# Kernel tuning notes

Hardware: AMD Instinct MI355X
Metric: run time of the kernel (lower is better)

Reference implementation:

```python
import jax, jax.numpy as jnp
import numpy as np
import math

T, P, ITERS, H = 6, 8, 2, 8          # nr_types, num_proto, iters, n_head
D, F = 512, 1024                      # dim_proto, feature_dim (hidden_dim==D)
L = T * ITERS                         # 12 cross-attention layers


def _ln(x, g=None, b=None, eps=1e-5):
    m = x.mean(-1, keepdims=True)
    v = x.var(-1, keepdims=True)
    y = (x - m) * jax.lax.rsqrt(v + eps)
    if g is not None:
        y = y * g + b
    return y


def _forward(x_batch, batch_mask, node_type, pm_W, pm_b, pm_g, pm_bn,
             proto_logsigma, rand_mul, Wq, bq, Wk, bk, Wv, bv, Wo, bo,
             ag, ab, Wm1, bm1, lg, lb, Wm2, bm2, pg, pb):
    B, N, _ = x_batch.shape
    dt = x_batch.dtype
    bm = batch_mask.astype(dt)                                   # [B,N]
    onehot = jax.nn.one_hot(node_type, T, dtype=dt)              # [B,N,T]
    valid = bm * jnp.any(x_batch != 0, axis=-1).astype(dt)       # [B,N]
    mbt = onehot * valid[:, :, None]                             # [B,N,T]
    sums = jnp.einsum('bnt,bnf->btf', mbt, x_batch)              # per-(batch,type) sum
    cnt = mbt.sum(1)                                             # [B,T]
    fallback = x_batch.sum(1) / bm.sum(1, keepdims=True)         # [B,F]
    proto_mu = jnp.where(cnt[..., None] > 0,
                         sums / jnp.maximum(cnt, 1.0)[..., None],
                         fallback[:, None, :])                   # [B,T,F]

    # proto_mlp: Linear + LayerNorm + GELU (dropout = eval/identity)
    mu = jax.nn.gelu(_ln(proto_mu @ pm_W + pm_b, pm_g, pm_bn), approximate=False)  # [B,T,D]
    all_proto = mu[:, :, None, :] + jnp.exp(proto_logsigma)[None] * rand_mul[None]  # [B,T,P,D]

    dh = D // H
    scale = 1.0 / math.sqrt(dh)
    keymask = bm[:, None, None, :] == 0                          # [B,1,1,N]

    def layer(q, i):
        resid = q                                                 # [B,P,D]
        k = _ln((x_batch @ Wk[i] + bk[i]).reshape(B, N, H, dh))   # QK-LayerNorm (no affine)
        v = (x_batch @ Wv[i] + bv[i]).reshape(B, N, H, dh)
        qh = _ln((q @ Wq[i] + bq[i]).reshape(B, P, H, dh))
        dots = jnp.einsum('bkhd,bnhd->bkhn', qh, k) * scale       # [B,P,H,N]
        dots = jnp.where(keymask, -jnp.inf, dots)
        attn = jax.nn.softmax(dots, axis=-1)
        upd = jnp.einsum('bnhd,bkhn->bkhd', v, attn).reshape(B, P, D)
        upd = upd @ Wo[i] + bo[i]
        q = resid + _ln(upd, ag[i], ab[i])
        h = jax.nn.gelu(_ln(q @ Wm1[i] + bm1[i], lg[i], lb[i]), approximate=False)
        h = h @ Wm2[i] + bm2[i]
        return q + _ln(h, pg[i], pb[i])

    outs = []
    c = 0
    for i in range(T):
        p = all_proto[:, i]
        for _ in range(ITERS):
            p = layer(p, c)
            c += 1
        outs.append(p)
    prototypes = jnp.stack(outs, axis=1)                          # [B,T,P,D]
    return prototypes, proto_mu


def setup_inputs() -> dict:
    key = jax.random.key(0)
    ks = jax.random.split(key, 40)
    B, N = 4, 4096
    sc = 0.02

    def rn(i, shape, s=sc):
        return jax.random.normal(ks[i], shape, jnp.float32) * s

    inp = {
        'x_batch': jax.random.normal(ks[0], (B, N, F), jnp.float32),
        'batch_mask': jax.random.randint(ks[1], (B, N), 0, 2, jnp.int32),
        'node_type': jax.random.randint(ks[2], (B, N), 0, T, jnp.int32),
        'pm_W': rn(3, (F, D)), 'pm_b': jnp.zeros((D,)),
        'pm_g': jnp.ones((D,)), 'pm_bn': jnp.zeros((D,)),
        'proto_logsigma': rn(4, (T, 1, D), 0.05),
        'rand_mul': jax.random.normal(ks[5], (T, P, D), jnp.float32),
        'Wq': rn(6, (L, D, D)), 'bq': jnp.zeros((L, D)),
        'Wk': rn(7, (L, F, D)), 'bk': jnp.zeros((L, D)),
        'Wv': rn(8, (L, F, D)), 'bv': jnp.zeros((L, D)),
        'Wo': rn(9, (L, D, D)), 'bo': jnp.zeros((L, D)),
        'ag': jnp.ones((L, D)), 'ab': jnp.zeros((L, D)),
        'Wm1': rn(10, (L, D, D)), 'bm1': jnp.zeros((L, D)),
        'lg': jnp.ones((L, D)), 'lb': jnp.zeros((L, D)),
        'Wm2': rn(11, (L, D, D)), 'bm2': jnp.zeros((L, D)),
        'pg': jnp.ones((L, D)), 'pb': jnp.zeros((L, D)),
    }
    return inp


def reference(x_batch, batch_mask, node_type, pm_W, pm_b, pm_g, pm_bn,
              proto_logsigma, rand_mul, Wq, bq, Wk, bk, Wv, bv, Wo, bo,
              ag, ab, Wm1, bm1, lg, lb, Wm2, bm2, pg, pb):
    return _forward(x_batch, batch_mask, node_type, pm_W, pm_b, pm_g, pm_bn,
                    proto_logsigma, rand_mul, Wq, bq, Wk, bk, Wv, bv, Wo, bo,
                    ag, ab, Wm1, bm1, lg, lb, Wm2, bm2, pg, pb)
```

## Files before the change

### kernel.cpp

```cpp
#include <hip/hip_runtime.h>
#include <hip/hip_bf16.h>
#include <stdint.h>

#define TT 6
#define PP 8
#define HH 8
#define DD 512
#define FF 1024
#define DH 64
#define NB 4
#define NN 4096
#define LL 12
#define NCH 16
#define CHK 256

typedef __attribute__((ext_vector_type(8))) short short8v;
typedef __attribute__((ext_vector_type(4))) float f32x4;
typedef __attribute__((ext_vector_type(4))) unsigned short u16x4;
typedef __attribute__((ext_vector_type(8))) unsigned short u16x8;
typedef unsigned short u16;

__device__ __forceinline__ float bf2f(u16 u){
  union { unsigned int i; float f; } x; x.i = ((unsigned int)u) << 16; return x.f;
}
// ... 224 lines not shown
    pref[0] = 0;
    for (int j = 0; j < 256; ++j) pref[j+1] = pref[j] + csum[j];
  }
  __syncthreads();
  int off = b*NN + pref[tid];
  #pragma unroll
  for (int i = 0; i < 16; ++i){ if (f[i]) nidx[off++] = tid*16 + i; }
  if (tid == 0) cntc[b] = pref[256];
}

__global__ void k_wbfT(const void* __restrict__ Wq, const void* __restrict__ Wo,
                       const void* __restrict__ Wm1, const void* __restrict__ Wm2,
                       u16* __restrict__ Wt, const int* __restrict__ flagp){
  int f32 = *flagp;
  int z = blockIdx.z;
  int fam = z / LL;
  const void* src = (fam==0) ? Wq : (fam==1) ? Wo : (fam==2) ? Wm1 : Wm2;
  size_t sbase = (size_t)(z % LL) * DD * DD;
  __shared__ u16 tile[32][33];
  int d0 = blockIdx.x*32, k0 = blockIdx.y*32;
  int tx = threadIdx.x, ty = threadIdx.y;
  #pragma unroll
  for (int i = 0; i < 4; ++i){
    size_t idx = sbase + (size_t)(k0 + ty + i*8)*DD + d0 + tx;
    u16 v;
    if (f32) v = f2bf(((const float*)src)[idx]);
    else     v = ((const u16*)src)[idx];
    tile[ty + i*8][tx] = v;
  }
  __syncthreads();
  #pragma unroll
  for (int i = 0; i < 4; ++i)
    Wt[((size_t)z*DD + d0 + ty + i*8)*DD + k0 + tx] = tile[tx][ty + i*8];
}

__global__ void __launch_bounds__(512) k_mu(const float* __restrict__ colsums,
   const float* __restrict__ coltotal, const float* __restrict__ cnt,
   const float* __restrict__ bmsum,
   const void* __restrict__ pmWx, const void* __restrict__ pmb,
   const void* __restrict__ pmg, const void* __restrict__ pmbn,
   const void* __restrict__ lsig, const void* __restrict__ rmul,
   float* __restrict__ qstate, void* __restrict__ dout, int wmode,
   const int* __restrict__ flagp){
  int f32 = *flagp;
  int wf32 = wmode ? f32 : 0;
  const size_t OFFP = (size_t)NB*TT*PP*DD;
  int bt = blockIdx.x; int b = bt/TT, t = bt%TT;
  int d = threadIdx.x;
  __shared__ float xs[FF];
  __shared__ float red[4096];
  __shared__ float r1[8], r2[8];
  float cv = cnt[bt];
  float inv = 1.f / fmaxf(cv, 1.f);
  float fbinv = 1.f / bmsum[b];
  #pragma unroll
  for (int h = 0; h < 2; ++h){
    int f = d + h*512;
    float pm = (cv > 0.f) ? colsums[(size_t)bt*FF + f] * inv
                          : coltotal[b*FF + f] * fbinv;
    xs[f] = pm;
    if (f32) ((float*)dout)[OFFP + (size_t)bt*FF + f] = pm;
    else     ((u16*)dout)[OFFP + (size_t)bt*FF + f] = f2bf(pm);
  }
  __syncthreads();
  float acc = ldf(pmb, d, f32) + gemv_vec(xs, pmWx, 0, FF, wf32, red, d);
  int lane = d & 63, wid = d >> 6;
  float s1 = wave_sum(acc), s2 = wave_sum(acc*acc);
  if (lane==0){ r1[wid]=s1; r2[wid]=s2; }
  __syncthreads();
  float m=0, qq=0;
  #pragma unroll
  for (int i=0;i<8;++i){ m+=r1[i]; qq+=r2[i]; }
  m *= (1.f/DD); float var = qq*(1.f/DD) - m*m;
  float y = (acc - m) * rsqrtf(var + 1e-5f) * ldf(pmg, d, f32) + ldf(pmbn, d, f32);
  float mu = 0.5f * y * (1.f + erff(y * 0.70710678118654752f));
  #pragma unroll
  for (int p = 0; p < PP; ++p){
    float rv = ldf(rmul, (size_t)(t*PP+p)*DD + d, f32);
    float ls = ldf(lsig, (size_t)t*DD + d, f32);
    qstate[(((size_t)(b*TT+t))*PP + p)*DD + d] = mu + expf(ls) * rv;
  }
}

__global__ void k_transpose(const void* __restrict__ Wk, const void* __restrict__ Wv,
                            u16* __restrict__ TK, u16* __restrict__ TV,
                            int tlo, int s, const int* __restrict__ flagp){
  int f32 = *flagp;
  int ti = blockIdx.z >> 1, kv = blockIdx.z & 1;
  int c = 2*(tlo+ti)+s;
  size_t eoff = (size_t)c*FF*DD;
  const void* W = kv ? Wv : Wk;
  u16* T = (kv ? TV : TK) + (size_t)ti*FF*DD;
  __shared__ u16 tile[32][33];
  int n0 = blockIdx.x * 32, k0 = blockIdx.y * 32;
  int tx = threadIdx.x, ty = threadIdx.y;
  #pragma unroll
  for (int i = 0; i < 4; ++i){
    size_t idx = eoff + (size_t)(k0 + ty + i*8)*DD + n0 + tx;
    u16 v;
    if (f32) v = f2bf(((const float*)W)[idx]);
    else     v = ((const u16*)W)[idx];
    tile[ty + i*8][tx] = v;
  }
  __syncthreads();
  #pragma unroll
  for (int i = 0; i < 4; ++i)
    T[(size_t)(n0 + ty + i*8)*FF + k0 + tx] = tile[tx][ty + i*8];
}

__global__ void __launch_bounds__(512) k_kvgemm(const u16* __restrict__ Xb,
    const u16* __restrict__ TK, const u16* __restrict__ TV,
    const void* __restrict__ bk, const void* __restrict__ bv,
    u16* __restrict__ Kb, u16* __restrict__ Vb,
    const int* __restrict__ nidx, const int* __restrict__ cntc,
    int tlo, int s, int nt, const int* __restrict__ flagp){
  int f32 = *flagp;
  int orig = blockIdx.x;
  int x = orig & 7, r = orig >> 3;
  int bx = r / nt, pr = r - bx*nt;
  int pairg = x*nt + pr;
  int by = pairg & 3; int kvti = pairg >> 2; int kv = kvti & 1; int ti = kvti >> 1;
  int b = bx >> 4, jt = bx & 15;
  int cnt = cntc[b];
  if (jt*256 >= cnt) return;
  int c = 2*(tlo+ti)+s;
  size_t boff = (size_t)c*DD;
  const u16* WT = (kv ? TV : TK) + (size_t)ti*FF*DD;
  const void* bias = kv ? bv : bk;
  u16* out = (kv ? Vb : Kb) + (size_t)ti*((size_t)NB*NN*DD);
  int n0 = by*128;
  __shared__ __align__(16) char LDS[3*24576];
  int tid = threadIdx.x, wid = tid >> 6, lane = tid & 63;
  int wr = wid >> 1, wcn = wid & 1;
  const u16* gp0; const u16* gp1; const u16* gp2;
  int lo0, lo1, lo2;
  {
    const u16* gps[3]; int los[3];
    #pragma unroll
    for (int i = 0; i < 3; ++i){
      int e = tid + i*512;
      if (e < 1024){
        int row = e>>2, sp = e&3;
        int ssrc = sp ^ (((row>>3)&1)<<1);
        int cl = jt*256 + row; if (cl >= cnt) cl = cnt-1;
        int grow = nidx[b*NN + cl];
        gps[i] = Xb + ((size_t)b*NN + grow)*FF + ssrc*8;
        los[i] = e*16;
      } else {
        int e2 = e - 1024;
        int row = e2>>2, sp = e2&3;
        int ssrc = sp ^ (((row>>3)&1)<<1);
        gps[i] = WT + (size_t)(n0 + row)*FF + ssrc*8;
        los[i] = 16384 + e2*16;
      }
    }
    gp0=gps[0]; gp1=gps[1]; gp2=gps[2];
    lo0=los[0]; lo1=los[1]; lo2=los[2];
  }
#define STAGE(T) { char* bb_ = LDS + ((T)%3)*24576; \
  glds16(gp0 + (T)*32, bb_ + lo0); glds16(gp1 + (T)*32, bb_ + lo1); \
  glds16(gp2 + (T)*32, bb_ + lo2); }
  int ke = (lane>>4) ^ (((lane>>3)&1)<<1);
  int arow[4], brow[4];
  #pragma unroll
  for (int mi = 0; mi < 4; ++mi)
    arow[mi] = (wr*64 + mi*16 + (lane&15))*64 + ke*16;
  #pragma unroll
  for (int ni = 0; ni < 4; ++ni)
    brow[ni] = 16384 + (wcn*64 + ni*16 + (lane&15))*64 + ke*16;
  f32x4 acc[4][4] = {};
  STAGE(0);
  STAGE(1);
  asm volatile("s_waitcnt vmcnt(3)" ::: "memory");
  __builtin_amdgcn_sched_barrier(0);
  __builtin_amdgcn_s_barrier();
  __builtin_amdgcn_sched_barrier(0);
  #pragma unroll
  for (int t = 0; t < 32; ++t){
    const char* Bbuf = LDS + (t%3)*24576;
    short8v af[4], bf[4];
    #pragma unroll
    for (int mi = 0; mi < 4; ++mi)
      af[mi] = *(const short8v*)(Bbuf + arow[mi]);
    #pragma unroll
    for (int ni = 0; ni < 4; ++ni)
      bf[ni] = *(const short8v*)(Bbuf + brow[ni]);
    if (t + 2 <= 31) STAGE(t+2);
    __builtin_amdgcn_s_setprio(1);
    #pragma unroll
    for (int mi = 0; mi < 4; ++mi)
      #pragma unroll
      for (int ni = 0; ni < 4; ++ni)
        acc[mi][ni] = __builtin_amdgcn_mfma_f32_16x16x32_bf16(af[mi], bf[ni], acc[mi][ni], 0, 0, 0);
    __builtin_amdgcn_s_setprio(0);
    if (t < 30)       asm volatile("s_waitcnt vmcnt(3)" ::: "memory");
    else if (t == 30) asm volatile("s_waitcnt vmcnt(0)" ::: "memory");
    __builtin_amdgcn_sched_barrier(0);
    if (t < 31){
      __builtin_amdgcn_s_barrier();
      __builtin_amdgcn_sched_barrier(0);
    }
  }
#undef STAGE
  #pragma unroll
  for (int mi = 0; mi < 4; ++mi){
    #pragma unroll
    for (int ni = 0; ni < 4; ++ni){
      int col = n0 + wcn*64 + ni*16 + (lane & 15);
      int h = col >> 6, dh = col & 63;
      float bvf = ldf(bias, boff + col, f32);
      #pragma unroll
      for (int r2 = 0; r2 < 4; ++r2){
        int row = jt*256 + wr*64 + mi*16 + (lane>>4)*4 + r2;
        out[(((size_t)(b*HH + h))*NN + row)*DH + dh] = f2bf(acc[mi][ni][r2] + bvf);
      }
    }
  }
}

__global__ void __launch_bounds__(512) k_qproj(const float* __restrict__ qstate,
      const void* __restrict__ Wq, const void* __restrict__ bq,
      float* __restrict__ qh, int tlo, int s, int wmode,
      const int* __restrict__ flagp){
  int f32 = *flagp;
  int wf32 = wmode ? f32 : 0;
  int z = blockIdx.x; int ti = z >> 5, rr = z & 31;
  int b = rr >> 3, p = rr & 7;
  int t = tlo + ti, c = 2*t + s;
  size_t woff = (size_t)c*DD*DD, boff = (size_t)c*DD;
  int d = threadIdx.x;
  __shared__ float xs[DD];
  __shared__ float red[4096];
  const float* xrow = qstate + (((size_t)(b*TT+t))*PP + p)*DD;
  xs[d] = xrow[d];
  __syncthreads();
  float acc = ldf(bq, boff + d, f32) + gemv_vec(xs, Wq, woff, DD, wf32, red, d);
  float s1 = wave_sum(acc) * (1.f/DH);
  float s2 = wave_sum(acc*acc) * (1.f/DH);
  float var = s2 - s1*s1;
  qh[(size_t)z*DD + d] = (acc - s1) * rsqrtf(var + 1e-5f);
}

__global__ void __launch_bounds__(512) k_attnA(const u16* __restrict__ Kb,
     const u16* __restrict__ Vb, const float* __restrict__ qh,
     const int* __restrict__ cntc, float* __restrict__ Opart, float* __restrict__ lpart){
  int ic = blockIdx.x, bh = blockIdx.y, ti = blockIdx.z;
  int b = bh >> 3, h = bh & 7;
  int cnt = cntc[b];
  if (ic*CHK >= cnt) return;
  int tid = threadIdx.x, p8 = tid >> 6, ln = tid & 63;
  int r8 = ln >> 3, g = ln & 7;
  __shared__ __align__(16) char KV[32768];
  __shared__ float qs[PP*DH];
  __shared__ float qsum[PP];
  __shared__ float e_lds[CHK*9];
  int rem = cnt - ic*CHK;
  float qv = qh[((size_t)(ti*32 + b*PP + p8))*DD + h*DH + ln];
  size_t tioff = (size_t)ti*((size_t)NB*NN*DD);
  const u16* Kbase = Kb + tioff + ((size_t)(b*HH + h)*NN + (size_t)ic*CHK)*DH;
  const u16* Vbase = Vb + tioff + ((size_t)(b*HH + h)*NN + (size_t)ic*CHK)*DH;
  #pragma unroll
  for (int i = 0; i < 4; ++i){
    int e = tid + i*512;
    int row = e >> 3, sp = e & 7;
    int ss = sp ^ (row & 7);
    int rr = row < rem ? row : rem-1;
    glds16(Vbase + (size_t)rr*DH + ss*8, (char*)KV + e*16);
  }
  qs[p8*DH + ln] = qv;
  {
    float sQ = wave_sum(qv);
    if (ln == 0) qsum[p8] = sQ;
  }
  asm volatile("s_waitcnt lgkmcnt(0)" ::: "memory");
  __builtin_amdgcn_sched_barrier(0);
  __builtin_amdgcn_s_barrier();
  __builtin_amdgcn_sched_barrier(0);
  #pragma unroll
  for (int it = 0; it < CHK/64; ++it){
    int nl = it*64 + p8*8 + r8;
    int rr8 = nl < rem ? nl : rem-1;
    u16x8 kv8 = *(const u16x8*)(Kbase + (size_t)rr8*DH + g*8);
    float kf[8];
    #pragma unroll
    for (int e = 0; e < 8; ++e) kf[e] = bf2f(kv8[e]);
    float sm = 0, sq = 0;
    #pragma unroll
    for (int e = 0; e < 8; ++e){ sm += kf[e]; sq += kf[e]*kf[e]; }
    #pragma unroll
    for (int o = 1; o < 8; o <<= 1){
      sm += __shfl_xor(sm, o);
      sq += __shfl_xor(sq, o);
    }
    sm *= (1.f/DH); sq = sq*(1.f/DH) - sm*sm;
    float inv = rsqrtf(sq + 1e-5f);
    float ap[8];
    #pragma unroll
    for (int p = 0; p < 8; ++p){
      f32x4 qa = *(const f32x4*)&qs[p*DH + g*8];
      f32x4 qb = *(const f32x4*)&qs[p*DH + g*8 + 4];
      ap[p] = kf[0]*qa.x + kf[1]*qa.y + kf[2]*qa.z + kf[3]*qa.w
            + kf[4]*qb.x + kf[5]*qb.y + kf[6]*qb.z + kf[7]*qb.w;
    }
    #pragma unroll
    for (int o = 1; o < 8; o <<= 1){
      #pragma unroll
      for (int p = 0; p < 8; ++p) ap[p] += __shfl_xor(ap[p], o);
    }
    float dg = (g==0)?ap[0]:(g==1)?ap[1]:(g==2)?ap[2]:(g==3)?ap[3]
             : (g==4)?ap[4]:(g==5)?ap[5]:(g==6)?ap[6]:ap[7];
    float sv = (dg - sm*qsum[g]) * inv * 0.125f;
    e_lds[nl*9 + g] = (nl < rem) ? __expf(sv) : 0.f;
  }
  __syncthreads();
  {
    float lp = 0;
    #pragma unroll
    for (int j = 0; j < CHK/64; ++j) lp += e_lds[(ln + j*64)*9 + p8];
    lp = wave_sum(lp);
    if (ln == 0) lpart[((size_t)(ti*32+bh)*NCH + ic)*PP + p8] = lp;
  }
  {
    float a0=0,a1=0,a2=0,a3=0,a4=0,a5=0,a6=0,a7=0;
    int vseg = (r8 ^ g) * 16;
    #pragma unroll 4
    for (int m = 0; m < CHK/8; ++m){
      float e = e_lds[(g + m*8)*9 + p8];
      u16x8 vv = *(const u16x8*)((const char*)KV + (g + m*8)*128 + vseg);
      a0 += e*bf2f(vv[0]); a1 += e*bf2f(vv[1]);
      a2 += e*bf2f(vv[2]); a3 += e*bf2f(vv[3]);
      a4 += e*bf2f(vv[4]); a5 += e*bf2f(vv[5]);
      a6 += e*bf2f(vv[6]); a7 += e*bf2f(vv[7]);
    }
    #pragma unroll
    for (int o = 1; o < 8; o <<= 1){
      a0 += __shfl_xor(a0, o); a1 += __shfl_xor(a1, o);
      a2 += __shfl_xor(a2, o); a3 += __shfl_xor(a3, o);
      a4 += __shfl_xor(a4, o); a5 += __shfl_xor(a5, o);
      a6 += __shfl_xor(a6, o); a7 += __shfl_xor(a7, o);
    }
    if (g == 0){
      float* op = Opart + ((size_t)(ti*32+bh)*NCH + ic)*512 + p8*64 + r8*8;
      f32x4 lo = {a0,a1,a2,a3}, hi = {a4,a5,a6,a7};
      *(f32x4*)op = lo;
      *((f32x4*)op + 1) = hi;
    }
  }
}

__global__ void __launch_bounds__(512) k_tailm(
    const float* __restrict__ Opart, const float* __restrict__ lpart,
    const int* __restrict__ cntc,
    float* __restrict__ qstate, float* __restrict__ qh,
    const u16* __restrict__ Wt,
    const void* __restrict__ bo, const void* __restrict__ ag, const void* __restrict__ ab,
    const void* __restrict__ bm1, const void* __restrict__ lg, const void* __restrict__ lb,
    const void* __restrict__ bm2, const void* __restrict__ pg, const void* __restrict__ pb,
    const void* __restrict__ bq, void* __restrict__ dout,
    int tlo, int s, int nt, const int* __restrict__ flagp){
  int f32 = *flagp;
  int ti = blockIdx.x & 7, b = blockIdx.x >> 3;
  if (ti >= nt) return;
  int t = tlo + ti, c = 2*t + s;
  int tid = threadIdx.x;
  int w = tid >> 6, lane = tid & 63, q4 = lane >> 4, l15 = lane & 15;
  int n0w = w*64;
  size_t boff = (size_t)c*DD;
  const size_t famSz = (size_t)LL*DD*DD;
  __shared__ u16 As[16*520];
  __shared__ float red1[128], red2[128];
  __shared__ float lval[64];
  int nch = (cntc[b] + CHK - 1) / CHK;
  for (int i = tid; i < 16*520; i += 512) As[i] = 0;
  if (tid < 64){
    int p = tid >> 3, hh = tid & 7;
    float l = 0;
    for (int ic = 0; ic < nch; ++ic)
      l += lpart[((size_t)(ti*32 + b*8 + hh)*NCH + ic)*PP + p];
    lval[tid] = 1.f / l;
  }
  __syncthreads();
  {
    int hh = tid >> 6, dd = tid & 63;
    #pragma unroll
    for (int p = 0; p < 8; ++p){
      float o = 0;
      for (int ic = 0; ic < nch; ++ic)
        o += Opart[((size_t)(ti*32 + b*8 + hh)*NCH + ic)*512 + p*64 + dd];
      As[p*520 + hh*64 + dd] = f2bf(o * lval[p*8 + hh]);
    }
  }
  __syncthreads();
  f32x4 acc[4], q2[4];
  float mv[4], rv[4];
  size_t qoffb = ((size_t)(b*TT+t))*PP*DD;
  {
    const u16* Bp = Wt + famSz + (size_t)c*DD*DD;
    tail_gemm8(acc, Bp, As, l15, q4, n0w);
    #pragma unroll
    for (int ni = 0; ni < 4; ++ni){
      float bv = ldf(bo, boff + n0w + ni*16 + l15, f32);
      #pragma unroll
      for (int r = 0; r < 4; ++r) acc[ni][r] += bv;
    }
    row_ln8(acc, red1, red2, w, l15, q4, mv, rv);
    #pragma unroll
    for (int ni = 0; ni < 4; ++ni){
      int col = n0w + ni*16 + l15;
      float gm = ldf(ag, boff + col, f32), bt = ldf(ab, boff + col, f32);
      #pragma unroll
      for (int r = 0; r < 4; ++r){
        int row = q4*4 + r;
        float y = (acc[ni][r] - mv[r])*rv[r]*gm + bt;
        float res = (q4 < 2) ? qstate[qoffb + (size_t)row*DD + col] : 0.f;
        q2[ni][r] = res + y;
      }
    }
    if (q4 < 2){
      #pragma unroll
      for (int r = 0; r < 4; ++r){
        int row = q4*4 + r;
        #pragma unroll
        for (int ni = 0; ni < 4; ++ni)
          As[row*520 + n0w + ni*16 + l15] = f2bf(q2[ni][r]);
      }
    }
  }
  __syncthreads();
  {
    const u16* Bp = Wt + 2*famSz + (size_t)c*DD*DD;
    tail_gemm8(acc, Bp, As, l15, q4, n0w);
    #pragma unroll
    for (int ni = 0; ni < 4; ++ni){
      float bv = ldf(bm1, boff + n0w + ni*16 + l15, f32);
      #pragma unroll
      for (int r = 0; r < 4; ++r) acc[ni][r] += bv;
    }
    row_ln8(acc, red1, red2, w, l15, q4, mv, rv);
    #pragma unroll
    for (int ni = 0; ni < 4; ++ni){
      int col = n0w + ni*16 + l15;
      float gm = ldf(lg, boff + col, f32), bt = ldf(lb, boff + col, f32);
      #pragma unroll
      for (int r = 0; r < 4; ++r){
        int row = q4*4 + r;
        float y = (acc[ni][r] - mv[r])*rv[r]*gm + bt;
        y = 0.5f*y*(1.f + erff(y*0.70710678118654752f));
        if (q4 < 2) As[row*520 + col] = f2bf(y);
      }
    }
  }
  __syncthreads();
  {
    const u16* Bp = Wt + 3*famSz + (size_t)c*DD*DD;
    tail_gemm8(acc, Bp, As, l15, q4, n0w);
    #pragma unroll
    for (int ni = 0; ni < 4; ++ni){
      float bv = ldf(bm2, boff + n0w + ni*16 + l15, f32);
      #pragma unroll
      for (int r = 0; r < 4; ++r) acc[ni][r] += bv;
    }
    row_ln8(acc, red1, red2, w, l15, q4, mv, rv);
    #pragma unroll
    for (int ni = 0; ni < 4; ++ni){
      int col = n0w + ni*16 + l15;
      float gm = ldf(pg, boff + col, f32), bt = ldf(pb, boff + col, f32);
      #pragma unroll
      for (int r = 0; r < 4; ++r){
        int row = q4*4 + r;
        float outv = q2[ni][r] + (acc[ni][r] - mv[r])*rv[r]*gm + bt;
        if (q4 < 2){
          qstate[qoffb + (size_t)row*DD + col] = outv;
          if (s == 0) As[row*520 + col] = f2bf(outv);
          else {
            if (f32) ((float*)dout)[qoffb + (size_t)row*DD + col] = outv;
            else     ((u16*)dout)[qoffb + (size_t)row*DD + col] = f2bf(outv);
          }
        }
      }
    }
  }
  if (s == 0){
    __syncthreads();
    const u16* Bp = Wt + (size_t)(c+1)*DD*DD;
    tail_gemm8(acc, Bp, As, l15, q4, n0w);
    #pragma unroll
    for (int ni = 0; ni < 4; ++ni){
      float bv = ldf(bq, (size_t)(c+1)*DD + n0w + ni*16 + l15, f32);
      #pragma unroll
      for (int r = 0; r < 4; ++r) acc[ni][r] += bv;
    }
    float s1[4], s2[4];
    #pragma unroll
    for (int r = 0; r < 4; ++r){
      float a0=acc[0][r], a1=acc[1][r], a2=acc[2][r], a3=acc[3][r];
      s1[r] = (a0+a1)+(a2+a3);
      s2[r] = (a0*a0+a1*a1)+(a2*a2+a3*a3);
    }
    #pragma unroll
    for (int o = 1; o < 16; o <<= 1)
      #pragma unroll
      for (int r = 0; r < 4; ++r){
        s1[r] += __shfl_xor(s1[r], o);
        s2[r] += __shfl_xor(s2[r], o);
      }
    if (q4 < 2){
      #pragma unroll
      for (int r = 0; r < 4; ++r){
        int row = q4*4 + r;
        float m = s1[r] * (1.f/DH);
        float var = s2[r] * (1.f/DH) - m*m;
        float ri = rsqrtf(var + 1e-5f);
        #pragma unroll
        for (int ni = 0; ni < 4; ++ni){
          int col = n0w + ni*16 + l15;
          qh[((size_t)(ti*32 + b*8 + row))*DD + col] = (acc[ni][r] - m)*ri;
        }
      }
    }
  }
}

__global__ void __launch_bounds__(512) k_tail(
    const float* __restrict__ Opart, const float* __restrict__ lpart,
    const int* __restrict__ cntc,
    float* __restrict__ qstate, float* __restrict__ qh,
    const void* __restrict__ Wo_, const void* __restrict__ Wm1_,
    const void* __restrict__ Wm2_, const void* __restrict__ Wq_,
    const void* __restrict__ bo, const void* __restrict__ ag, const void* __restrict__ ab,
    const void* __restrict__ bm1, const void* __restrict__ lg, const void* __restrict__ lb,
    const void* __restrict__ bm2, const void* __restrict__ pg, const void* __restrict__ pb,
    const void* __restrict__ bq,
    int tlo, int s, int wmode, const int* __restrict__ flagp){
  int f32 = *flagp;
  int wf32 = wmode ? f32 : 0;
  int z = blockIdx.x; int ti = z >> 5, rr = z & 31;
  int b = rr >> 3, p = rr & 7;
  int t = tlo + ti, c = 2*t + s;
  int d = threadIdx.x;
  int h = d >> 6, dd = d & 63;
  int lane = d & 63, wid = d >> 6;
  size_t qoff = (((size_t)(b*TT+t))*PP + p)*DD;
  size_t boff = (size_t)c*DD;
  size_t w0 = (size_t)c*DD*DD;
  __shared__ float xs[DD];
  __shared__ float red[4096];
  __shared__ float r1[8], r2[8];
  int nch = (cntc[b] + CHK - 1) / CHK;
  float o = 0, l = 0;
  for (int ic = 0; ic < nch; ++ic){
    o += Opart[((size_t)(ti*32 + b*8 + h)*NCH + ic)*512 + p*64 + dd];
    l += lpart[((size_t)(ti*32 + b*8 + h)*NCH + ic)*PP + p];
  }
  float upd = o / l;
  xs[d] = upd;
  __syncthreads();
  float acc = ldf(bo, boff + d, f32) + gemv_vec(xs, Wo_, w0, DD, wf32, red, d);
  {
    float s1 = wave_sum(acc), s2 = wave_sum(acc*acc);
    if (lane == 0){ r1[wid] = s1; r2[wid] = s2; }
  }
  __syncthreads();
  float m = 0, qv = 0;
  #pragma unroll
  for (int i = 0; i < 8; ++i){ m += r1[i]; qv += r2[i]; }
  m *= (1.f/DD); float var = qv*(1.f/DD) - m*m;
  float y = (acc - m)*rsqrtf(var + 1e-5f)*ldf(ag, boff+d, f32) + ldf(ab, boff+d, f32);
  float q2 = qstate[qoff + d] + y;
  __syncthreads();
  xs[d] = q2;
  __syncthreads();
  float acc2 = ldf(bm1, boff + d, f32) + gemv_vec(xs, Wm1_, w0, DD, wf32, red, d);
  {
    float s1 = wave_sum(acc2), s2 = wave_sum(acc2*acc2);
    if (lane == 0){ r1[wid] = s1; r2[wid] = s2; }
  }
  __syncthreads();
  m = 0; qv = 0;
  #pragma unroll
  for (int i = 0; i < 8; ++i){ m += r1[i]; qv += r2[i]; }
  m *= (1.f/DD); var = qv*(1.f/DD) - m*m;
  float y2 = (acc2 - m)*rsqrtf(var + 1e-5f)*ldf(lg, boff+d, f32) + ldf(lb, boff+d, f32);
  y2 = 0.5f*y2*(1.f + erff(y2*0.70710678118654752f));
  __syncthreads();
  xs[d] = y2;
  __syncthreads();
  float acc3 = ldf(bm2, boff + d, f32) + gemv_vec(xs, Wm2_, w0, DD, wf32, red, d);
  {
    float s1 = wave_sum(acc3), s2 = wave_sum(acc3*acc3);
    if (lane == 0){ r1[wid] = s1; r2[wid] = s2; }
  }
  __syncthreads();
  m = 0; qv = 0;
  #pragma unroll
  for (int i = 0; i < 8; ++i){ m += r1[i]; qv += r2[i]; }
  m *= (1.f/DD); var = qv*(1.f/DD) - m*m;
  float y3 = (acc3 - m)*rsqrtf(var + 1e-5f)*ldf(pg, boff+d, f32) + ldf(pb, boff+d, f32);
  float outv = q2 + y3;
  qstate[qoff + d] = outv;
  if (s == 0){
    __syncthreads();
    xs[d] = outv;
    __syncthreads();
    size_t w1 = (size_t)(c+1)*DD*DD;
    float accq = ldf(bq, (size_t)(c+1)*DD + d, f32) + gemv_vec(xs, Wq_, w1, DD, wf32, red, d);
    float t1 = wave_sum(accq) * (1.f/DH);
    float t2 = wave_sum(accq*accq) * (1.f/DH);
    float var2 = t2 - t1*t1;
    qh[(size_t)z*DD + d] = (accq - t1) * rsqrtf(var2 + 1e-5f);
  }
}

__global__ void k_out(const float* __restrict__ qstate, void* __restrict__ dout,
                      const int* __restrict__ flagp){
  int f32 = *flagp;
  int i = blockIdx.x*256 + threadIdx.x;
  if (f32) ((float*)dout)[i] = qstate[i];
  else     ((u16*)dout)[i] = f2bf(qstate[i]);
}

extern "C" void kernel_launch(void* const* d_in, const int* in_sizes, int n_in,
                              void* d_out, int out_size, void* d_ws, size_t ws_size,
                              hipStream_t stream){
  (void)in_sizes; (void)n_in; (void)out_size;
  const void* X   = d_in[0];
  const int* bm    = (const int*)d_in[1];
  const int* ntype = (const int*)d_in[2];
  const void* pmW = d_in[3];  const void* pmb = d_in[4];
  const void* pmg = d_in[5];  const void* pmbn= d_in[6];
  const void* lsig= d_in[7];  const void* rmul= d_in[8];
  const void* Wq  = d_in[9];  const void* bq  = d_in[10];
  const void* Wk  = d_in[11]; const void* bk  = d_in[12];
  const void* Wv  = d_in[13]; const void* bv  = d_in[14];
  const void* Wo  = d_in[15]; const void* bo  = d_in[16];
  const void* ag  = d_in[17]; const void* ab  = d_in[18];
  const void* Wm1 = d_in[19]; const void* bm1 = d_in[20];
  const void* lg  = d_in[21]; const void* lb  = d_in[22];
  const void* Wm2 = d_in[23]; const void* bm2 = d_in[24];
  const void* pg  = d_in[25]; const void* pb  = d_in[26];

  char* ws = (char*)d_ws;
  int*   flagp    = (int*)(ws + 0);
  float* cnt      = (float*)(ws + 256);
  float* bmsum    = (float*)(ws + 512);
  float* colsums  = (float*)(ws + 768);
  float* coltotal = (float*)(ws + 99072);
  float* qstate   = (float*)(ws + 279296);
  int*   cntc     = (int*)(ws + 672512);
  int*   nidx     = (int*)(ws + 672768);

  size_t off = 738304;
  auto take = [&](size_t bytes)->char*{
    char* p = ws + off; off = (off + bytes + 255) & ~(size_t)255; return p;
  };
  u16* Xbf = (u16*)take((size_t)NB*NN*FF*2);

  const size_t perT = (size_t)65536
                    + 16384
                    + 1048576
                    + 2*1048576
                    + 2*16777216;
  size_t base = off;
  int nt = 1;
  if      (ws_size >= base + 6*perT + 65536) nt = 6;
  else if (ws_size >= base + 3*perT + 65536) nt = 3;
  else if (ws_size >= base + 2*perT + 65536) nt = 2;

  float* qh    = (float*)take((size_t)nt*65536);
  float* lpart = (float*)take((size_t)nt*16384);
  float* Opart = (float*)take((size_t)nt*1048576);
  u16*   WkT   = (u16*)take((size_t)nt*1048576);
  u16*   WvT   = (u16*)take((size_t)nt*1048576);
  u16*   Kb    = (u16*)take((size_t)nt*16777216);
  u16*   Vb    = (u16*)take((size_t)nt*16777216);

  const size_t wtBytes = (size_t)4*LL*DD*DD*2;
  int useWt = (ws_size >= off + wtBytes + 65536) ? 1 : 0;
  u16* Wt = useWt ? (u16*)take(wtBytes) : nullptr;

  const size_t pmwbB = (size_t)FF*DD*2;
  const size_t wqbB  = (size_t)LL*DD*DD*2;
  int useCvt = (ws_size >= off + pmwbB + wqbB + 65536) ? 1 : 0;
  u16* pmWb = useCvt ? (u16*)take(pmwbB) : nullptr;
  u16* Wqb  = useCvt ? (u16*)take(wqbB)  : nullptr;

  hipMemsetAsync(ws + 256, 0, 115200, stream);
  k_detect<<<1, 256, 0, stream>>>(X, flagp);
  k_compact<<<NB, 256, 0, stream>>>(bm, nidx, cntc);
  if (useWt)
    k_wbfT<<<dim3(16, 16, 4*LL), dim3(32, 8), 0, stream>>>(Wq, Wo, Wm1, Wm2, Wt, flagp);
  if (useCvt){
    const int n0q = (FF*DD)/4;
    const int nblk = (FF*DD + LL*DD*DD)/4/256;
    k_cvt2<<<nblk, 256, 0, stream>>>(pmW, pmWb, n0q, Wq, Wqb, flagp);
  }
  k_xcv<<<dim3(64, NB), 256, 0, stream>>>(X, Xbf, bm, ntype, colsums, coltotal,
                                          cnt, bmsum, flagp);
  if (useCvt)
    k_mu<<<NB*TT, 512, 0, stream>>>(colsums, coltotal, cnt, bmsum,
        pmWb, pmb, pmg, pmbn, lsig, rmul, qstate, d_out, 0, flagp);
  else
    k_mu<<<NB*TT, 512, 0, stream>>>(colsums, coltotal, cnt, bmsum,
        pmW, pmb, pmg, pmbn, lsig, rmul, qstate, d_out, 1, flagp);

  for (int tlo = 0; tlo < TT; tlo += nt){
    for (int s = 0; s < 2; ++s){
      k_transpose<<<dim3(16, 32, 2*nt), dim3(32, 8), 0, stream>>>(
          Wk, Wv, WkT, WvT, tlo, s, flagp);
      k_kvgemm<<<64*8*nt, 512, 0, stream>>>(
          Xbf, WkT, WvT, bk, bv, Kb, Vb, nidx, cntc, tlo, s, nt, flagp);
      if (s == 0){
        if (useCvt)
          k_qproj<<<nt*32, 512, 0, stream>>>(qstate, Wqb, bq, qh, tlo, s, 0, flagp);
        else
          k_qproj<<<nt*32, 512, 0, stream>>>(qstate, Wq, bq, qh, tlo, s, 1, flagp);
      }
      k_attnA<<<dim3(NCH, 32, nt), 512, 0, stream>>>(Kb, Vb, qh, cntc, Opart, lpart);
      if (useWt)
        k_tailm<<<32, 512, 0, stream>>>(Opart, lpart, cntc, qstate, qh, Wt,
            bo, ag, ab, bm1, lg, lb, bm2, pg, pb, bq, d_out, tlo, s, nt, flagp);
      else
        k_tail<<<nt*32, 512, 0, stream>>>(Opart, lpart, cntc, qstate, qh,
            Wo, Wm1, Wm2, Wq, bo, ag, ab, bm1, lg, lb, bm2, pg, pb, bq,
            tlo, s, 1, flagp);
    }
  }
  if (!useWt)
    k_out<<<NB*TT*PP*DD/256, 256, 0, stream>>>(qstate, d_out, flagp);
}
```

Before: 647.8 us.

## Co-schedule qproj and tail MLP with KV GEMM in fused launches

Both sub-layers' Wk/Wv transposes now run in a single launch, which needs a double-sized transpose buffer. The q-projection is merged into the first K/V GEMM launch. The second sub-layer's K/V GEMM shares a launch with the first sub-layer's tail MLP, with block index choosing the role. Kernel bodies become device functions that use a shared LDS buffer. The aim is to hide the small, low-occupancy qproj and tail kernels behind the large GEMM and to cut launch count. The cost is a larger workspace per type, which could lower nt when the workspace is tight.

New measurement: 699.9 us. 1.08x slower.

```diff
diff --git a/kernel.cpp b/kernel.cpp
--- a/kernel.cpp
+++ b/kernel.cpp
@@ -330,15 +330,18 @@
   }
 }
 
-__global__ void k_transpose(const void* __restrict__ Wk, const void* __restrict__ Wv,
-                            u16* __restrict__ TK, u16* __restrict__ TV,
-                            int tlo, int s, const int* __restrict__ flagp){
+__global__ void k_transpose2(const void* __restrict__ Wk, const void* __restrict__ Wv,
+                             u16* __restrict__ TK, u16* __restrict__ TV,
+                             int tlo, int nt, const int* __restrict__ flagp){
   int f32 = *flagp;
-  int ti = blockIdx.z >> 1, kv = blockIdx.z & 1;
-  int c = 2*(tlo+ti)+s;
+  int z = blockIdx.z;
+  int kv = z & 1, q = z >> 1;
+  int si = (q >= nt) ? 1 : 0;
+  int ti = q - si*nt;
+  int c = 2*(tlo+ti)+si;
   size_t eoff = (size_t)c*FF*DD;
   const void* W = kv ? Wv : Wk;
-  u16* T = (kv ? TV : TK) + (size_t)ti*FF*DD;
+  u16* T = (kv ? TV : TK) + (size_t)q*FF*DD;
   __shared__ u16 tile[32][33];
   int n0 = blockIdx.x * 32, k0 = blockIdx.y * 32;
   int tx = threadIdx.x, ty = threadIdx.y;
@@ -356,14 +359,12 @@
     T[(size_t)(n0 + ty + i*8)*FF + k0 + tx] = tile[tx][ty + i*8];
 }
 
-__global__ void __launch_bounds__(512) k_kvgemm(const u16* __restrict__ Xb,
-    const u16* __restrict__ TK, const u16* __restrict__ TV,
+__device__ __forceinline__ void kvgemm_body(char* LDS, int orig,
+    const u16* __restrict__ Xb, const u16* __restrict__ TK, const u16* __restrict__ TV,
     const void* __restrict__ bk, const void* __restrict__ bv,
     u16* __restrict__ Kb, u16* __restrict__ Vb,
     const int* __restrict__ nidx, const int* __restrict__ cntc,
-    int tlo, int s, int nt, const int* __restrict__ flagp){
-  int f32 = *flagp;
-  int orig = blockIdx.x;
+    int tlo, int s, int nt, int f32){
   int x = orig & 7, r = orig >> 3;
   int bx = r / nt, pr = r - bx*nt;
   int pairg = x*nt + pr;
@@ -373,11 +374,10 @@
   if (jt*256 >= cnt) return;
   int c = 2*(tlo+ti)+s;
   size_t boff = (size_t)c*DD;
-  const u16* WT = (kv ? TV : TK) + (size_t)ti*FF*DD;
+  const u16* WT = (kv ? TV : TK) + (size_t)(s*nt + ti)*FF*DD;
   const void* bias = kv ? bv : bk;
   u16* out = (kv ? Vb : Kb) + (size_t)ti*((size_t)NB*NN*DD);
   int n0 = by*128;
-  __shared__ __align__(16) char LDS[3*24576];
   int tid = threadIdx.x, wid = tid >> 6, lane = tid & 63;
   int wr = wid >> 1, wcn = wid & 1;
   const u16* gp0; const u16* gp1; const u16* gp2;
@@ -466,19 +466,18 @@
   }
 }
 
-__global__ void __launch_bounds__(512) k_qproj(const float* __restrict__ qstate,
-      const void* __restrict__ Wq, const void* __restrict__ bq,
-      float* __restrict__ qh, int tlo, int s, int wmode,
-      const int* __restrict__ flagp){
-  int f32 = *flagp;
+__device__ __forceinline__ void qproj_body(char* LDSb, int z,
+      const float* __restrict__ qstate, const void* __restrict__ Wq,
+      const void* __restrict__ bq, float* __restrict__ qh,
+      int tlo, int wmode, int f32){
   int wf32 = wmode ? f32 : 0;
-  int z = blockIdx.x; int ti = z >> 5, rr = z & 31;
+  int ti = z >> 5, rr = z & 31;
   int b = rr >> 3, p = rr & 7;
-  int t = tlo + ti, c = 2*t + s;
+  int t = tlo + ti, c = 2*t;
   size_t woff = (size_t)c*DD*DD, boff = (size_t)c*DD;
   int d = threadIdx.x;
-  __shared__ float xs[DD];
-  __shared__ float red[4096];
+  float* xs  = (float*)LDSb;
+  float* red = (float*)(LDSb + 2048);
   const float* xrow = qstate + (((size_t)(b*TT+t))*PP + p)*DD;
   xs[d] = xrow[d];
   __syncthreads();
@@ -487,6 +486,255 @@
   float s2 = wave_sum(acc*acc) * (1.f/DH);
   float var = s2 - s1*s1;
   qh[(size_t)z*DD + d] = (acc - s1) * rsqrtf(var + 1e-5f);
+}
+
+__device__ __forceinline__ void tailm_body(char* LDSb, int idx,
+    const float* __restrict__ Opart, const float* __restrict__ lpart,
+    const int* __restrict__ cntc,
+    float* __restrict__ qstate, float* __restrict__ qh,
+    const u16* __restrict__ Wt,
+    const void* __restrict__ bo, const void* __restrict__ ag, const void* __restrict__ ab,
+    const void* __restrict__ bm1, const void* __restrict__ lg, const void* __restrict__ lb,
+    const void* __restrict__ bm2, const void* __restrict__ pg, const void* __restrict__ pb,
+    const void* __restrict__ bq, void* __restrict__ dout,
+    int tlo, int s, int nt, int f32){
+  int ti = idx & 7, b = idx >> 3;
+  if (ti >= nt) return;
+  int t = tlo + ti, c = 2*t + s;
+  int tid = threadIdx.x;
+  int w = tid >> 6, lane = tid & 63, q4 = lane >> 4, l15 = lane & 15;
+  int n0w = w*64;
+  size_t boff = (size_t)c*DD;
+  const size_t famSz = (size_t)LL*DD*DD;
+  u16*   As   = (u16*)LDSb;
+  float* red1 = (float*)(LDSb + 16640);
+  float* red2 = (float*)(LDSb + 17152);
+  float* lval = (float*)(LDSb + 17664);
+  int nch = (cntc[b] + CHK - 1) / CHK;
+  for (int i = tid; i < 16*520; i += 512) As[i] = 0;
+  if (tid < 64){
+    int p = tid >> 3, hh = tid & 7;
+    float l = 0;
+    for (int ic = 0; ic < nch; ++ic)
+      l += lpart[((size_t)(ti*32 + b*8 + hh)*NCH + ic)*PP + p];
+    lval[tid] = 1.f / l;
+  }
+  __syncthreads();
+  {
+    int hh = tid >> 6, dd = tid & 63;
+    #pragma unroll
+    for (int p = 0; p < 8; ++p){
+      float o = 0;
+      for (int ic = 0; ic < nch; ++ic)
+        o += Opart[((size_t)(ti*32 + b*8 + hh)*NCH + ic)*512 + p*64 + dd];
+      As[p*520 + hh*64 + dd] = f2bf(o * lval[p*8 + hh]);
+    }
+  }
+  __syncthreads();
+  f32x4 acc[4], q2[4];
+  float mv[4], rv[4];
+  size_t qoffb = ((size_t)(b*TT+t))*PP*DD;
+  {
+    const u16* Bp = Wt + famSz + (size_t)c*DD*DD;
+    tail_gemm8(acc, Bp, As, l15, q4, n0w);
+    #pragma unroll
+    for (int ni = 0; ni < 4; ++ni){
+      float bv = ldf(bo, boff + n0w + ni*16 + l15, f32);
+      #pragma unroll
+      for (int r = 0; r < 4; ++r) acc[ni][r] += bv;
+    }
+    row_ln8(acc, red1, red2, w, l15, q4, mv, rv);
+    #pragma unroll
+    for (int ni = 0; ni < 4; ++ni){
+      int col = n0w + ni*16 + l15;
+      float gm = ldf(ag, boff + col, f32), bt = ldf(ab, boff + col, f32);
+      #pragma unroll
+      for (int r = 0; r < 4; ++r){
+        int row = q4*4 + r;
+        float y = (acc[ni][r] - mv[r])*rv[r]*gm + bt;
+        float res = (q4 < 2) ? qstate[qoffb + (size_t)row*DD + col] : 0.f;
+        q2[ni][r] = res + y;
+      }
+    }
+    if (q4 < 2){
+      #pragma unroll
+      for (int r = 0; r < 4; ++r){
+        int row = q4*4 + r;
+        #pragma unroll
+        for (int ni = 0; ni < 4; ++ni)
+          As[row*520 + n0w + ni*16 + l15] = f2bf(q2[ni][r]);
+      }
+    }
+  }
+  __syncthreads();
+  {
+    const u16* Bp = Wt + 2*famSz + (size_t)c*DD*DD;
+    tail_gemm8(acc, Bp, As, l15, q4, n0w);
+    #pragma unroll
+    for (int ni = 0; ni < 4; ++ni){
+      float bv = ldf(bm1, boff + n0w + ni*16 + l15, f32);
+      #pragma unroll
+      for (int r = 0; r < 4; ++r) acc[ni][r] += bv;
+    }
+    row_ln8(acc, red1, red2, w, l15, q4, mv, rv);
+    #pragma unroll
+    for (int ni = 0; ni < 4; ++ni){
+      int col = n0w + ni*16 + l15;
+      float gm = ldf(lg, boff + col, f32), bt = ldf(lb, boff + col, f32);
+      #pragma unroll
+      for (int r = 0; r < 4; ++r){
+        int row = q4*4 + r;
+        float y = (acc[ni][r] - mv[r])*rv[r]*gm + bt;
+        y = 0.5f*y*(1.f + erff(y*0.70710678118654752f));
+        if (q4 < 2) As[row*520 + col] = f2bf(y);
+      }
+    }
+  }
+  __syncthreads();
+  {
+    const u16* Bp = Wt + 3*famSz + (size_t)c*DD*DD;
+    tail_gemm8(acc, Bp, As, l15, q4, n0w);
+    #pragma unroll
+    for (int ni = 0; ni < 4; ++ni){
+      float bv = ldf(bm2, boff + n0w + ni*16 + l15, f32);
+      #pragma unroll
+      for (int r = 0; r < 4; ++r) acc[ni][r] += bv;
+    }
+    row_ln8(acc, red1, red2, w, l15, q4, mv, rv);
+    #pragma unroll
+    for (int ni = 0; ni < 4; ++ni){
+      int col = n0w + ni*16 + l15;
+      float gm = ldf(pg, boff + col, f32), bt = ldf(pb, boff + col, f32);
+      #pragma unroll
+      for (int r = 0; r < 4; ++r){
+        int row = q4*4 + r;
+        float outv = q2[ni][r] + (acc[ni][r] - mv[r])*rv[r]*gm + bt;
+        if (q4 < 2){
+          qstate[qoffb + (size_t)row*DD + col] = outv;
+          if (s == 0) As[row*520 + col] = f2bf(outv);
+          else {
+            if (f32) ((float*)dout)[qoffb + (size_t)row*DD + col] = outv;
+            else     ((u16*)dout)[qoffb + (size_t)row*DD + col] = f2bf(outv);
+          }
+        }
+      }
+    }
+  }
+  if (s == 0){
+    __syncthreads();
+    const u16* Bp = Wt + (size_t)(c+1)*DD*DD;
+    tail_gemm8(acc, Bp, As, l15, q4, n0w);
+    #pragma unroll
+    for (int ni = 0; ni < 4; ++ni){
+      float bv = ldf(bq, (size_t)(c+1)*DD + n0w + ni*16 + l15, f32);
+      #pragma unroll
+      for (int r = 0; r < 4; ++r) acc[ni][r] += bv;
+    }
+    float s1[4], s2[4];
+    #pragma unroll
+    for (int r = 0; r < 4; ++r){
+      float a0=acc[0][r], a1=acc[1][r], a2=acc[2][r], a3=acc[3][r];
+      s1[r] = (a0+a1)+(a2+a3);
+      s2[r] = (a0*a0+a1*a1)+(a2*a2+a3*a3);
+    }
+    #pragma unroll
+    for (int o = 1; o < 16; o <<= 1)
+      #pragma unroll
+      for (int r = 0; r < 4; ++r){
+        s1[r] += __shfl_xor(s1[r], o);
+        s2[r] += __shfl_xor(s2[r], o);
+      }
+    if (q4 < 2){
+      #pragma unroll
+      for (int r = 0; r < 4; ++r){
+        int row = q4*4 + r;
+        float m = s1[r] * (1.f/DH);
+        float var = s2[r] * (1.f/DH) - m*m;
+        float ri = rsqrtf(var + 1e-5f);
+        #pragma unroll
+        for (int ni = 0; ni < 4; ++ni){
+          int col = n0w + ni*16 + l15;
+          qh[((size_t)(ti*32 + b*8 + row))*DD + col] = (acc[ni][r] - m)*ri;
+        }
+      }
+    }
+  }
+}
+
+__global__ void __launch_bounds__(512) k_kvgemm(const u16* __restrict__ Xb,
+    const u16* __restrict__ TK, const u16* __restrict__ TV,
+    const void* __restrict__ bk, const void* __restrict__ bv,
+    u16* __restrict__ Kb, u16* __restrict__ Vb,
+    const int* __restrict__ nidx, const int* __restrict__ cntc,
+    int tlo, int s, int nt, const int* __restrict__ flagp){
+  __shared__ __align__(16) char LDS[73728];
+  kvgemm_body(LDS, blockIdx.x, Xb, TK, TV, bk, bv, Kb, Vb, nidx, cntc,
+              tlo, s, nt, *flagp);
+}
+
+__global__ void __launch_bounds__(512) k_qproj(const float* __restrict__ qstate,
+      const void* __restrict__ Wq, const void* __restrict__ bq,
+      float* __restrict__ qh, int tlo, int wmode,
+      const int* __restrict__ flagp){
+  __shared__ __align__(16) char LDSb[18432];
+  qproj_body(LDSb, blockIdx.x, qstate, Wq, bq, qh, tlo, wmode, *flagp);
+}
+
+__global__ void __launch_bounds__(512) k_tailm(
+    const float* __restrict__ Opart, const float* __restrict__ lpart,
+    const int* __restrict__ cntc,
+    float* __restrict__ qstate, float* __restrict__ qh,
+    const u16* __restrict__ Wt,
+    const void* __restrict__ bo, const void* __restrict__ ag, const void* __restrict__ ab,
+    const void* __restrict__ bm1, const void* __restrict__ lg, const void* __restrict__ lb,
+    const void* __restrict__ bm2, const void* __restrict__ pg, const void* __restrict__ pb,
+    const void* __restrict__ bq, void* __restrict__ dout,
+    int tlo, int s, int nt, const int* __restrict__ flagp){
+  __shared__ __align__(16) char LDSb[17920];
+  tailm_body(LDSb, blockIdx.x, Opart, lpart, cntc, qstate, qh, Wt,
+             bo, ag, ab, bm1, lg, lb, bm2, pg, pb, bq, dout, tlo, s, nt, *flagp);
+}
+
+__global__ void __launch_bounds__(512) k_kvq(const u16* __restrict__ Xb,
+    const u16* __restrict__ TK, const u16* __restrict__ TV,
+    const void* __restrict__ bk, const void* __restrict__ bv,
+    u16* __restrict__ Kb, u16* __restrict__ Vb,
+    const int* __restrict__ nidx, const int* __restrict__ cntc,
+    const float* __restrict__ qstate, const void* __restrict__ Wq,
+    const void* __restrict__ bq, float* __restrict__ qh,
+    int tlo, int nt, int wmode, int nq, const int* __restrict__ flagp){
+  __shared__ __align__(16) char LDS[73728];
+  int f32 = *flagp;
+  if ((int)blockIdx.x < nq)
+    qproj_body(LDS, blockIdx.x, qstate, Wq, bq, qh, tlo, wmode, f32);
+  else
+    kvgemm_body(LDS, blockIdx.x - nq, Xb, TK, TV, bk, bv, Kb, Vb, nidx, cntc,
+                tlo, 0, nt, f32);
+}
+
+__global__ void __launch_bounds__(512) k_tmkv(
+    const float* __restrict__ Opart, const float* __restrict__ lpart,
+    const int* __restrict__ cntc,
+    float* __restrict__ qstate, float* __restrict__ qh,
+    const u16* __restrict__ Wt,
+    const void* __restrict__ bo, const void* __restrict__ ag, const void* __restrict__ ab,
+    const void* __restrict__ bm1, const void* __restrict__ lg, const void* __restrict__ lb,
+    const void* __restrict__ bm2, const void* __restrict__ pg, const void* __restrict__ pb,
+    const void* __restrict__ bq, void* __restrict__ dout,
+    const u16* __restrict__ Xb,
+    const u16* __restrict__ TK, const u16* __restrict__ TV,
+    const void* __restrict__ bk, const void* __restrict__ bv,
+    u16* __restrict__ Kb, u16* __restrict__ Vb,
+    const int* __restrict__ nidx,
+    int tlo, int nt, const int* __restrict__ flagp){
+  __shared__ __align__(16) char LDS[73728];
+  int f32 = *flagp;
+  if (blockIdx.x < 32)
+    tailm_body(LDS, blockIdx.x, Opart, lpart, cntc, qstate, qh, Wt,
+               bo, ag, ab, bm1, lg, lb, bm2, pg, pb, bq, dout, tlo, 0, nt, f32);
+  else
+    kvgemm_body(LDS, blockIdx.x - 32, Xb, TK, TV, bk, bv, Kb, Vb, nidx, cntc,
+                tlo, 1, nt, f32);
 }
 
 __global__ void __launch_bounds__(512) k_attnA(const u16* __restrict__ Kb,
@@ -592,179 +840,6 @@
       f32x4 lo = {a0,a1,a2,a3}, hi = {a4,a5,a6,a7};
       *(f32x4*)op = lo;
       *((f32x4*)op + 1) = hi;
-    }
-  }
-}
-
-__global__ void __launch_bounds__(512) k_tailm(
-    const float* __restrict__ Opart, const float* __restrict__ lpart,
-    const int* __restrict__ cntc,
-    float* __restrict__ qstate, float* __restrict__ qh,
-    const u16* __restrict__ Wt,
-    const void* __restrict__ bo, const void* __restrict__ ag, const void* __restrict__ ab,
-    const void* __restrict__ bm1, const void* __restrict__ lg, const void* __restrict__ lb,
-    const void* __restrict__ bm2, const void* __restrict__ pg, const void* __restrict__ pb,
-    const void* __restrict__ bq, void* __restrict__ dout,
-    int tlo, int s, int nt, const int* __restrict__ flagp){
-  int f32 = *flagp;
-  int ti = blockIdx.x & 7, b = blockIdx.x >> 3;
-  if (ti >= nt) return;
-  int t = tlo + ti, c = 2*t + s;
-  int tid = threadIdx.x;
-  int w = tid >> 6, lane = tid & 63, q4 = lane >> 4, l15 = lane & 15;
-  int n0w = w*64;
-  size_t boff = (size_t)c*DD;
-  const size_t famSz = (size_t)LL*DD*DD;
-  __shared__ u16 As[16*520];
-  __shared__ float red1[128], red2[128];
-  __shared__ float lval[64];
-  int nch = (cntc[b] + CHK - 1) / CHK;
-  for (int i = tid; i < 16*520; i += 512) As[i] = 0;
-  if (tid < 64){
-    int p = tid >> 3, hh = tid & 7;
-    float l = 0;
-    for (int ic = 0; ic < nch; ++ic)
-      l += lpart[((size_t)(ti*32 + b*8 + hh)*NCH + ic)*PP + p];
-    lval[tid] = 1.f / l;
-  }
-  __syncthreads();
-  {
-    int hh = tid >> 6, dd = tid & 63;
-    #pragma unroll
-    for (int p = 0; p < 8; ++p){
-      float o = 0;
-      for (int ic = 0; ic < nch; ++ic)
-        o += Opart[((size_t)(ti*32 + b*8 + hh)*NCH + ic)*512 + p*64 + dd];
-      As[p*520 + hh*64 + dd] = f2bf(o * lval[p*8 + hh]);
-    }
-  }
-  __syncthreads();
-  f32x4 acc[4], q2[4];
-  float mv[4], rv[4];
-  size_t qoffb = ((size_t)(b*TT+t))*PP*DD;
-  {
-    const u16* Bp = Wt + famSz + (size_t)c*DD*DD;
-    tail_gemm8(acc, Bp, As, l15, q4, n0w);
-    #pragma unroll
-    for (int ni = 0; ni < 4; ++ni){
-      float bv = ldf(bo, boff + n0w + ni*16 + l15, f32);
-      #pragma unroll
-      for (int r = 0; r < 4; ++r) acc[ni][r] += bv;
-    }
-    row_ln8(acc, red1, red2, w, l15, q4, mv, rv);
-    #pragma unroll
-    for (int ni = 0; ni < 4; ++ni){
-      int col = n0w + ni*16 + l15;
-      float gm = ldf(ag, boff + col, f32), bt = ldf(ab, boff + col, f32);
-      #pragma unroll
-      for (int r = 0; r < 4; ++r){
-        int row = q4*4 + r;
-        float y = (acc[ni][r] - mv[r])*rv[r]*gm + bt;
-        float res = (q4 < 2) ? qstate[qoffb + (size_t)row*DD + col] : 0.f;
-        q2[ni][r] = res + y;
-      }
-    }
-    if (q4 < 2){
-      #pragma unroll
-      for (int r = 0; r < 4; ++r){
-        int row = q4*4 + r;
-        #pragma unroll
-        for (int ni = 0; ni < 4; ++ni)
-          As[row*520 + n0w + ni*16 + l15] = f2bf(q2[ni][r]);
-      }
-    }
-  }
-  __syncthreads();
-  {
-    const u16* Bp = Wt + 2*famSz + (size_t)c*DD*DD;
-    tail_gemm8(acc, Bp, As, l15, q4, n0w);
-    #pragma unroll
-    for (int ni = 0; ni < 4; ++ni){
-      float bv = ldf(bm1, boff + n0w + ni*16 + l15, f32);
-      #pragma unroll
-      for (int r = 0; r < 4; ++r) acc[ni][r] += bv;
-    }
-    row_ln8(acc, red1, red2, w, l15, q4, mv, rv);
-    #pragma unroll
-    for (int ni = 0; ni < 4; ++ni){
-      int col = n0w + ni*16 + l15;
-      float gm = ldf(lg, boff + col, f32), bt = ldf(lb, boff + col, f32);
-      #pragma unroll
-      for (int r = 0; r < 4; ++r){
-        int row = q4*4 + r;
-        float y = (acc[ni][r] - mv[r])*rv[r]*gm + bt;
-        y = 0.5f*y*(1.f + erff(y*0.70710678118654752f));
-        if (q4 < 2) As[row*520 + col] = f2bf(y);
-      }
-    }
-  }
-  __syncthreads();
-  {
-    const u16* Bp = Wt + 3*famSz + (size_t)c*DD*DD;
-    tail_gemm8(acc, Bp, As, l15, q4, n0w);
-    #pragma unroll
-    for (int ni = 0; ni < 4; ++ni){
-      float bv = ldf(bm2, boff + n0w + ni*16 + l15, f32);
-      #pragma unroll
-      for (int r = 0; r < 4; ++r) acc[ni][r] += bv;
-    }
-    row_ln8(acc, red1, red2, w, l15, q4, mv, rv);
-    #pragma unroll
-    for (int ni = 0; ni < 4; ++ni){
-      int col = n0w + ni*16 + l15;
-      float gm = ldf(pg, boff + col, f32), bt = ldf(pb, boff + col, f32);
-      #pragma unroll
-      for (int r = 0; r < 4; ++r){
-        int row = q4*4 + r;
-        float outv = q2[ni][r] + (acc[ni][r] - mv[r])*rv[r]*gm + bt;
-        if (q4 < 2){
-          qstate[qoffb + (size_t)row*DD + col] = outv;
-          if (s == 0) As[row*520 + col] = f2bf(outv);
-          else {
-            if (f32) ((float*)dout)[qoffb + (size_t)row*DD + col] = outv;
-            else     ((u16*)dout)[qoffb + (size_t)row*DD + col] = f2bf(outv);
-          }
-        }
-      }
-    }
-  }
-  if (s == 0){
-    __syncthreads();
-    const u16* Bp = Wt + (size_t)(c+1)*DD*DD;
-    tail_gemm8(acc, Bp, As, l15, q4, n0w);
-    #pragma unroll
-    for (int ni = 0; ni < 4; ++ni){
-      float bv = ldf(bq, (size_t)(c+1)*DD + n0w + ni*16 + l15, f32);
-      #pragma unroll
-      for (int r = 0; r < 4; ++r) acc[ni][r] += bv;
-    }
-    float s1[4], s2[4];
-    #pragma unroll
-    for (int r = 0; r < 4; ++r){
-      float a0=acc[0][r], a1=acc[1][r], a2=acc[2][r], a3=acc[3][r];
-      s1[r] = (a0+a1)+(a2+a3);
-      s2[r] = (a0*a0+a1*a1)+(a2*a2+a3*a3);
-    }
-    #pragma unroll
-    for (int o = 1; o < 16; o <<= 1)
-      #pragma unroll
-      for (int r = 0; r < 4; ++r){
-        s1[r] += __shfl_xor(s1[r], o);
-        s2[r] += __shfl_xor(s2[r], o);
-      }
-    if (q4 < 2){
-      #pragma unroll
-      for (int r = 0; r < 4; ++r){
-        int row = q4*4 + r;
-        float m = s1[r] * (1.f/DH);
-        float var = s2[r] * (1.f/DH) - m*m;
-        float ri = rsqrtf(var + 1e-5f);
-        #pragma unroll
-        for (int ni = 0; ni < 4; ++ni){
-          int col = n0w + ni*16 + l15;
-          qh[((size_t)(ti*32 + b*8 + row))*DD + col] = (acc[ni][r] - m)*ri;
-        }
-      }
     }
   }
 }
@@ -906,7 +981,7 @@
   const size_t perT = (size_t)65536
                     + 16384
                     + 1048576
-                    + 2*1048576
+                    + 4*1048576
                     + 2*16777216;
   size_t base = off;
   int nt = 1;
@@ -917,8 +992,8 @@
   float* qh    = (float*)take((size_t)nt*65536);
   float* lpart = (float*)take((size_t)nt*16384);
   float* Opart = (float*)take((size_t)nt*1048576);
-  u16*   WkT   = (u16*)take((size_t)nt*1048576);
-  u16*   WvT   = (u16*)take((size_t)nt*1048576);
+  u16*   WkT   = (u16*)take((size_t)nt*2*1048576);
+  u16*   WvT   = (u16*)take((size_t)nt*2*1048576);
   u16*   Kb    = (u16*)take((size_t)nt*16777216);
   u16*   Vb    = (u16*)take((size_t)nt*16777216);
 
@@ -931,6 +1006,9 @@
   int useCvt = (ws_size >= off + pmwbB + wqbB + 65536) ? 1 : 0;
   u16* pmWb = useCvt ? (u16*)take(pmwbB) : nullptr;
   u16* Wqb  = useCvt ? (u16*)take(wqbB)  : nullptr;
+
+  const void* WqG = useCvt ? (const void*)Wqb : Wq;
+  int wmode = useCvt ? 0 : 1;
 
   hipMemsetAsync(ws + 256, 0, 115200, stream);
   k_detect<<<1, 256, 0, stream>>>(X, flagp);
@@ -951,26 +1029,33 @@
     k_mu<<<NB*TT, 512, 0, stream>>>(colsums, coltotal, cnt, bmsum,
         pmW, pmb, pmg, pmbn, lsig, rmul, qstate, d_out, 1, flagp);
 
+  const int nkv = 64*8*nt;
   for (int tlo = 0; tlo < TT; tlo += nt){
-    for (int s = 0; s < 2; ++s){
-      k_transpose<<<dim3(16, 32, 2*nt), dim3(32, 8), 0, stream>>>(
-          Wk, Wv, WkT, WvT, tlo, s, flagp);
-      k_kvgemm<<<64*8*nt, 512, 0, stream>>>(
-          Xbf, WkT, WvT, bk, bv, Kb, Vb, nidx, cntc, tlo, s, nt, flagp);
-      if (s == 0){
-        if (useCvt)
-          k_qproj<<<nt*32, 512, 0, stream>>>(qstate, Wqb, bq, qh, tlo, s, 0, flagp);
-        else
-          k_qproj<<<nt*32, 512, 0, stream>>>(qstate, Wq, bq, qh, tlo, s, 1, flagp);
-      }
+    k_transpose2<<<dim3(16, 32, 4*nt), dim3(32, 8), 0, stream>>>(
+        Wk, Wv, WkT, WvT, tlo, nt, flagp);
+    if (useWt){
+      k_kvq<<<nt*32 + nkv, 512, 0, stream>>>(
+          Xbf, WkT, WvT, bk, bv, Kb, Vb, nidx, cntc,
+          qstate, WqG, bq, qh, tlo, nt, wmode, nt*32, flagp);
       k_attnA<<<dim3(NCH, 32, nt), 512, 0, stream>>>(Kb, Vb, qh, cntc, Opart, lpart);
-      if (useWt)
-        k_tailm<<<32, 512, 0, stream>>>(Opart, lpart, cntc, qstate, qh, Wt,
-            bo, ag, ab, bm1, lg, lb, bm2, pg, pb, bq, d_out, tlo, s, nt, flagp);
-      else
+      k_tmkv<<<32 + nkv, 512, 0, stream>>>(
+          Opart, lpart, cntc, qstate, qh, Wt,
+          bo, ag, ab, bm1, lg, lb, bm2, pg, pb, bq, d_out,
+          Xbf, WkT, WvT, bk, bv, Kb, Vb, nidx, tlo, nt, flagp);
+      k_attnA<<<dim3(NCH, 32, nt), 512, 0, stream>>>(Kb, Vb, qh, cntc, Opart, lpart);
+      k_tailm<<<32, 512, 0, stream>>>(Opart, lpart, cntc, qstate, qh, Wt,
+          bo, ag, ab, bm1, lg, lb, bm2, pg, pb, bq, d_out, tlo, 1, nt, flagp);
+    } else {
+      for (int s = 0; s < 2; ++s){
+        k_kvgemm<<<nkv, 512, 0, stream>>>(
+            Xbf, WkT, WvT, bk, bv, Kb, Vb, nidx, cntc, tlo, s, nt, flagp);
+        if (s == 0)
+          k_qproj<<<nt*32, 512, 0, stream>>>(qstate, WqG, bq, qh, tlo, wmode, flagp);
+        k_attnA<<<dim3(NCH, 32, nt), 512, 0, stream>>>(Kb, Vb, qh, cntc, Opart, lpart);
         k_tail<<<nt*32, 512, 0, stream>>>(Opart, lpart, cntc, qstate, qh,
             Wo, Wm1, Wm2, Wq, bo, ag, ab, bm1, lg, lb, bm2, pg, pb, bq,
             tlo, s, 1, flagp);
+      }
     }
   }
   if (!useWt)
```
